# Kernel tuning notes

Measured on AMD Instinct MI355X. Metric: run time of the kernel, lower is better.

Reference implementation:

```python
import jax, jax.numpy as jnp
import numpy as np

B, C, L = 8, 512, 2048   # batch, input_dim (channels), sequence length
H = 8                    # multihead_cnt
K = 3                    # kernel_dim
DH = C // H              # per-head dim = 64
SCALE = 1.0 / float(np.sqrt(C))  # module divides by sqrt(input_dim), not sqrt(head_dim)


def _conv1d(x, w, b):
    # x: [B, C, L], w: [C_out, C_in, K], padding=1 keeps L
    y = jax.lax.conv_general_dilated(x, w, window_strides=(1,), padding=[(1, 1)],
                                     dimension_numbers=('NCH', 'OIH', 'NCH'))
    return y + b[None, :, None]


def setup_inputs() -> dict:
    key = jax.random.key(0)
    ks = jax.random.split(key, 7)
    x = jax.random.normal(ks[0], (B, C, L), dtype=jnp.float32)
    # xavier_normal_ std for Conv1d weight [C, C, K]: sqrt(2 / (fan_in + fan_out)), fan = C*K
    std = float(np.sqrt(2.0 / (C * K + C * K)))
    inp = {'x': x}
    for i in range(3):  # conv_cnt = 3 -> q, k, v convolutions
        inp[f'w{i}'] = jax.random.normal(ks[1 + 2 * i], (C, C, K), dtype=jnp.float32) * std
        inp[f'b{i}'] = jax.random.normal(ks[2 + 2 * i], (C,), dtype=jnp.float32) * 0.01
    return inp


def reference(x, w0, b0, w1, b1, w2, b2):
    # q, k, v projections via Conv1d (padding preserves length)
    q = _conv1d(x, w0, b0)  # [B, C, L]
    k = _conv1d(x, w1, b1)
    v = _conv1d(x, w2, b2)
    # torch.chunk along dim 1 == contiguous reshape into heads
    qh = q.reshape(B, H, DH, L)
    kh = k.reshape(B, H, DH, L)
    vh = v.reshape(B, H, DH, L)
    # scores = q^T k / sqrt(input_dim)  -> [B, H, L, L]
    scores = jnp.einsum('bhdl,bhdm->bhlm', qh, kh) * SCALE
    att = jax.nn.softmax(scores, axis=-1)
    # out = (att @ v^T)^T -> [B, H, DH, L]
    out = jnp.einsum('bhlm,bhdm->bhdl', att, vh)
    return out.reshape(B, C, L)
```

## Files before the change

kernel.cpp:

```cpp
#include <hip/hip_runtime.h>
#include <hip/hip_bf16.h>
#include <cstdint>

typedef unsigned short u16;
typedef short v8s __attribute__((ext_vector_type(8)));
typedef float v4f __attribute__((ext_vector_type(4)));
typedef u16 u16x8 __attribute__((ext_vector_type(8)));
typedef u16 u16x4 __attribute__((ext_vector_type(4)));

static constexpr int Bb = 8, Cc = 512, Ll = 2048, Hh = 8, Dh = 64;

__device__ __forceinline__ float bf2f(u16 u){
  unsigned x = ((unsigned)u) << 16; float f; __builtin_memcpy(&f, &x, 4); return f;
}
__device__ __forceinline__ u16 f2bf(float f){
  unsigned x; __builtin_memcpy(&x, &f, 4);
  x = (x + 0x7fffu + ((x >> 16) & 1u)) >> 16; return (u16)x;
}

__device__ __forceinline__ void async_cp16(const u16* g, u16* l){
  __builtin_amdgcn_global_load_lds(
      (const __attribute__((address_space(1))) unsigned int*)g,
      (__attribute__((address_space(3))) unsigned int*)l, 16, 0, 0);
}

#if __has_builtin(__builtin_amdgcn_exp2f)
#define EXP2F(x) __builtin_amdgcn_exp2f(x)
#else
#define EXP2F(x) exp2f(x)
#endif

__global__ __launch_bounds__(256) void detect_dtype(const u16* __restrict__ x, unsigned* __restrict__ flag){
  __shared__ int cnt;
  if (threadIdx.x == 0) cnt = 0;
  __syncthreads();
  int sane = 0;
  for (int i = threadIdx.x; i < 4096; i += 256){
    unsigned e = (x[2 * i] >> 7) & 0xFFu;
    sane += (e >= 90u && e <= 160u) ? 1 : 0;
  }
  atomicAdd(&cnt, sane);
  __syncthreads();
  if (threadIdx.x == 0) *flag = (cnt < 2458) ? 1u : 0u;
}

__global__ __launch_bounds__(256) void transpose_pad(const void* __restrict__ xv, const unsigned* __restrict__ flagp,
                                                     u16* __restrict__ xT){
  int b = blockIdx.z, ci0 = blockIdx.y * 64, l0 = blockIdx.x * 64;
  __shared__ u16 tb[64 * 72];
  const unsigned isf32 = *flagp;
  int t = threadIdx.x;
  int row = t >> 3, seg = t & 7;
  if (isf32){
    const float* xf = (const float*)xv;
    #pragma unroll
    for (int rnd = 0; rnd < 2; rnd++){
      int ci = row + rnd * 32;
      size_t off = ((size_t)(b * Cc + ci0 + ci)) * Ll + l0 + seg * 8;
      v4f a = *(const v4f*)(xf + off);
      v4f c4 = *(const v4f*)(xf + off + 4);
      #pragma unroll
      for (int j = 0; j < 4; j++) tb[(seg * 8 + j) * 72 + ci] = f2bf(a[j]);
      #pragma unroll
      for (int j = 0; j < 4; j++) tb[(seg * 8 + 4 + j) * 72 + ci] = f2bf(c4[j]);
    }
  } else {
    const u16* x = (const u16*)xv;
    #pragma unroll
    for (int rnd = 0; rnd < 2; rnd++){
      int ci = row + rnd * 32;
      u16x8 v = *(const u16x8*)(x + ((size_t)(b * Cc + ci0 + ci)) * Ll + l0 + seg * 8);
      #pragma unroll
      for (int j = 0; j < 8; j++) tb[(seg * 8 + j) * 72 + ci] = v[j];
    }
  }
  __syncthreads();
  #pragma unroll
  for (int rnd = 0; rnd < 2; rnd++){
    int l = row + rnd * 32;
    u16x8 v = *(const u16x8*)&tb[l * 72 + seg * 8];
    *(u16x8*)(xT + ((size_t)b * 2050 + 1 + l0 + l) * Cc + ci0 + seg * 8) = v;
  }
  if (blockIdx.x == 0 && t < 8){
    u16x8 z = {};
    *(u16x8*)(xT + ((size_t)b * 2050 + 0) * Cc + ci0 + t * 8) = z;
  }
  if (blockIdx.x == 31 && t < 8){
    u16x8 z = {};
    *(u16x8*)(xT + ((size_t)b * 2050 + 2049) * Cc + ci0 + t * 8) = z;
  }
}

__global__ __launch_bounds__(256) void pack_wb(const void* __restrict__ w0, const void* __restrict__ w1,
                                               const void* __restrict__ w2, const void* __restrict__ b0,
                                               const void* __restrict__ b1, const void* __restrict__ b2,
                                               const unsigned* __restrict__ flagp,
                                               u16* __restrict__ wp, u16* __restrict__ bb){
  int g = blockIdx.x * 256 + threadIdx.x;
  const unsigned isf32 = *flagp;
  if (g < 9 * 512 * 512){
    int ci = g & 511, co = (g >> 9) & 511, kc = g >> 18;
    int conv = kc / 3, k = kc - conv * 3;
    const void* w = (conv == 0) ? w0 : ((conv == 1) ? w1 : w2);
    size_t idx = (size_t)co * 1536 + ci * 3 + k;
    wp[g] = isf32 ? f2bf(((const float*)w)[idx]) : ((const u16*)w)[idx];
  } else {
    int g2 = g - 9 * 512 * 512;
    if (g2 < 1536){
      int conv = g2 >> 9, c = g2 & 511;
      const void* bsrc = (conv == 0) ? b0 : ((conv == 1) ? b1 : b2);
      bb[g2] = isf32 ? f2bf(((const float*)bsrc)[c]) : ((const u16*)bsrc)[c];
    }
  }
}

__global__ __launch_bounds__(256) void conv_gemm_fused(const u16* __restrict__ wp, const u16* __restrict__ xT,
                                                       const u16* __restrict__ bb, u16* __restrict__ qT,
                                                       u16* __restrict__ kT, u16* __restrict__ vN){
  int b = blockIdx.y, bx = blockIdx.x;
  int mt = bx >> 3, nt = bx & 7;
  int m0 = mt * 128, n0 = nt * 256;
  int conv = m0 >> 9;
  int co0 = m0 & 511;
  __shared__ u16 smem[12288 + 8256];
  u16* lA = smem;
  u16* lB = smem + 12288;
  int t = threadIdx.x, wave = t >> 6, lane = t & 63, quad = lane >> 4, lid = lane & 15;
  int wm = (wave >> 1) * 64, wn = (wave & 1) * 128;
  v4f acc[4][8] = {};
  const size_t xbase = (size_t)b * 2050 * Cc;

  for (int it = 0; it < 16; it++){
    int ci0 = it << 5;
    #pragma unroll
    for (int r = 0; r < 4; r++){
      int e = (r * 256 + t) * 8;
      int row = e >> 5, cio = e & 31;
      async_cp16(xT + xbase + (size_t)(n0 + row) * 512 + ci0 + cio, &lB[e]);
    }
    #pragma unroll
    for (int r = 0; r < 6; r++){
      int e = (r * 256 + t) * 8;
      int ks = e >> 12, rem = e & 4095, row = rem >> 5, cio = rem & 31;
      async_cp16(wp + ((size_t)((conv * 3 + ks) * 512 + co0 + row)) * 512 + ci0 + cio, &lA[e]);
    }
    if (t < 8){
      int hr = 256 + (t >> 2), cio = (t & 3) * 8;
      u16x8 hv = *(const u16x8*)(xT + xbase + (size_t)(n0 + hr) * 512 + ci0 + cio);
      *(u16x8*)&lB[hr * 32 + cio] = hv;
    }
    __syncthreads();
    #pragma unroll
    for (int ks = 0; ks < 3; ks++){
      v8s aF[4], bF[8];
      #pragma unroll
      for (int i = 0; i < 4; i++) aF[i] = *(const v8s*)&lA[ks * 4096 + (wm + i * 16 + lid) * 32 + quad * 8];
      #pragma unroll
      for (int j = 0; j < 8; j++) bF[j] = *(const v8s*)&lB[(wn + j * 16 + lid + ks) * 32 + quad * 8];
      #pragma unroll
      for (int i = 0; i < 4; i++)
        #pragma unroll
        for (int j = 0; j < 8; j++)
          acc[i][j] = __builtin_amdgcn_mfma_f32_16x16x32_bf16(aF[i], bF[j], acc[i][j], 0, 0, 0);
    }
    __syncthreads();
  }

  const float qsc = (float)(1.4426950408889634 / 22.627416997969522);
  if (conv < 2){
    u16* dst = (conv == 0) ? qT : kT;
    #pragma unroll
    for (int i = 0; i < 4; i++){
      int cog = m0 + wm + i * 16 + quad * 4;
      float bv[4];
      #pragma unroll
      for (int r = 0; r < 4; r++) bv[r] = bf2f(bb[cog + r]);
      int co = cog & 511;
      #pragma unroll
      for (int j = 0; j < 8; j++){
        int l = n0 + wn + j * 16 + lid;
        u16x4 pk;
        #pragma unroll
        for (int r = 0; r < 4; r++){
          float v = acc[i][j][r] + bv[r];
          if (conv == 0) v *= qsc;
          pk[r] = f2bf(v);
        }
        *(u16x4*)(dst + ((((size_t)b * Hh + (co >> 6)) * Ll + l) << 6) + (co & 63)) = pk;
      }
    }
  } else {
    u16* scr = smem;
    #pragma unroll
    for (int cs = 0; cs < 2; cs++){
      __syncthreads();
      #pragma unroll
      for (int i = 0; i < 4; i++){
        int cog = m0 + wm + i * 16 + quad * 4;
        float bv[4];
        #pragma unroll
        for (int r = 0; r < 4; r++) bv[r] = bf2f(bb[cog + r]);
        #pragma unroll
        for (int j = 0; j < 4; j++){
          int jj = cs * 4 + j;
          int lcl = (wave & 1) * 64 + j * 16 + lid;
          #pragma unroll
          for (int r = 0; r < 4; r++)
            scr[(wm + i * 16 + quad * 4 + r) * 130 + lcl] = f2bf(acc[i][jj][r] + bv[r]);
        }
      }
      __syncthreads();
      int row = t & 127, half = t >> 7;
      int co = co0 + row;
      size_t gb = (((size_t)b * Cc + co) << 11) + n0 + half * 128 + cs * 64;
      #pragma unroll
      for (int s = 0; s < 8; s++){
        u16x8 vv = *(const u16x8*)&scr[row * 130 + half * 64 + s * 8];
        *(u16x8*)(vN + gb + s * 8) = vv;
      }
    }
  }
}

__global__ __launch_bounds__(256) void attn_kernel(const u16* __restrict__ qT, const u16* __restrict__ kT,
                                                   const u16* __restrict__ vN, const unsigned* __restrict__ flagp,
                                                   void* __restrict__ outv){
  int bhx = blockIdx.x;
  int b = bhx >> 3, h = bhx & 7, l0 = blockIdx.y * 128;
  int t = threadIdx.x, w = t >> 6, lane = t & 63, quad = lane >> 4, lid = lane & 15;
  __shared__ u16 kls[128 * 72];
  __shared__ u16 vls[64 * 136];
  const unsigned isf32 = *flagp;
  const size_t bh = (size_t)b * Hh + h;

  int kadd[5], vadd[5];
  bool kval[5], vval[5];
  #pragma unroll
  for (int r = 0; r < 5; r++){
    int e = (r * 256 + t) * 8;
    kval[r] = e < 128 * 72;
    int slot = e / 72, off = e - slot * 72;
    int s5 = slot & 31;
    int m = (slot & ~31) | (((s5 >> 2) & 1) << 3) | (((s5 >> 3) & 1) << 4) | (((s5 >> 4) & 1) << 2) | (s5 & 3);
    kadd[r] = m * 64 + (off < 64 ? off : 0);
    vval[r] = e < 64 * 136;
    int d = e / 136, voff = e - d * 136;
    vadd[r] = d * Ll + (voff < 128 ? voff : 0);
  }
  const u16* kTb = kT + bh * Ll * 64;
  const u16* vNb = vN + ((size_t)(b * Cc + h * Dh)) * Ll;

  v8s qF[2][2];
  #pragma unroll
  for (int ci = 0; ci < 2; ci++)
    #pragma unroll
    for (int ks = 0; ks < 2; ks++)
      qF[ci][ks] = *(const v8s*)(qT + ((bh * Ll) + l0 + w * 32 + ci * 16 + lid) * 64 + ks * 32 + quad * 8);

  const v8s onesF = {0x3F80, 0x3F80, 0x3F80, 0x3F80, 0x3F80, 0x3F80, 0x3F80, 0x3F80};
  v4f o[2][4] = {};
  v4f o1[2] = {};

  for (int mt = 0; mt < 16; mt++){
    int m0 = mt * 128;
    const u16* kt = kTb + (size_t)m0 * 64;
    const u16* vt = vNb + m0;
    #pragma unroll
    for (int r = 0; r < 5; r++)
      if (kval[r]) async_cp16(kt + kadd[r], &kls[(r * 256 + t) * 8]);
    #pragma unroll
    for (int r = 0; r < 5; r++)
      if (vval[r]) async_cp16(vt + vadd[r], &vls[(r * 256 + t) * 8]);
    __syncthreads();

    v4f s[4][2][2] = {};
    #pragma unroll
    for (int ks = 0; ks < 2; ks++){
      v8s aF[4][2];
      #pragma unroll
      for (int c = 0; c < 4; c++)
        #pragma unroll
        for (int tt = 0; tt < 2; tt++)
          aF[c][tt] = *(const v8s*)&kls[(c * 32 + tt * 16 + lid) * 72 + ks * 32 + quad * 8];
      #pragma unroll
      for (int c = 0; c < 4; c++)
        #pragma unroll
        for (int tt = 0; tt < 2; tt++){
          s[c][tt][0] = __builtin_amdgcn_mfma_f32_16x16x32_bf16(aF[c][tt], qF[0][ks], s[c][tt][0], 0, 0, 0);
          s[c][tt][1] = __builtin_amdgcn_mfma_f32_16x16x32_bf16(aF[c][tt], qF[1][ks], s[c][tt][1], 0, 0, 0);
        }
    }

    #pragma unroll
    for (int c = 0; c < 4; c++){
      v8s aP[2];
      #pragma unroll
      for (int ci = 0; ci < 2; ci++){
        float p[8];
        #pragma unroll
        for (int tt = 0; tt < 2; tt++)
          #pragma unroll
          for (int r = 0; r < 4; r++)
            p[tt * 4 + r] = EXP2F(s[c][tt][ci][r]);
        unsigned u[4];
        #pragma unroll
        for (int k2 = 0; k2 < 4; k2++){
          __hip_bfloat162 hb = __float22bfloat162_rn(make_float2(p[2 * k2], p[2 * k2 + 1]));
          __builtin_memcpy(&u[k2], &hb, 4);
        }
        __builtin_memcpy(&aP[ci], u, 16);
      }
      v8s bV[4];
      #pragma unroll
      for (int df = 0; df < 4; df++)
        bV[df] = *(const v8s*)&vls[(df * 16 + lid) * 136 + c * 32 + quad * 8];
      #pragma unroll
      for (int ci = 0; ci < 2; ci++){
        #pragma unroll
        for (int df = 0; df < 4; df++)
          o[ci][df] = __builtin_amdgcn_mfma_f32_16x16x32_bf16(aP[ci], bV[df], o[ci][df], 0, 0, 0);
        o1[ci] = __builtin_amdgcn_mfma_f32_16x16x32_bf16(aP[ci], onesF, o1[ci], 0, 0, 0);
      }
    }
    __syncthreads();
  }

  #pragma unroll
  for (int lf = 0; lf < 2; lf++){
    v4f nv;
    #pragma unroll
    for (int r = 0; r < 4; r++) nv[r] = 1.f / o1[lf][r];
    #pragma unroll
    for (int df = 0; df < 4; df++){
      int d = df * 16 + lid;
      int l = l0 + w * 32 + lf * 16 + quad * 4;
      size_t ofs = (((bh << 6) + d) << 11) + l;
      if (isf32){
        v4f st;
        #pragma unroll
        for (int r = 0; r < 4; r++) st[r] = o[lf][df][r] * nv[r];
        *(v4f*)((float*)outv + ofs) = st;
      } else {
        u16x4 pk;
        #pragma unroll
        for (int r = 0; r < 4; r++) pk[r] = f2bf(o[lf][df][r] * nv[r]);
        *(u16x4*)((u16*)outv + ofs) = pk;
      }
    }
  }
}

extern "C" void kernel_launch(void* const* d_in, const int* in_sizes, int n_in,
                              void* d_out, int out_size, void* d_ws, size_t ws_size,
                              hipStream_t stream){
  const void* x  = d_in[0];
  const void* w0 = d_in[1];
  const void* b0 = d_in[2];
  const void* w1 = d_in[3];
  const void* b1 = d_in[4];
  const void* w2 = d_in[5];
  const void* b2 = d_in[6];
  u16* ws = (u16*)d_ws;
  unsigned* flag = (unsigned*)ws;
  u16* xT = ws + 64;
  u16* wp = xT + (size_t)8 * 2050 * 512;
  u16* bb = wp + (size_t)9 * 512 * 512;
  u16* qT = bb + 1536;
  u16* kT = qT + (size_t)8 * 8 * 2048 * 64;
  u16* vN = kT + (size_t)8 * 8 * 2048 * 64;

  detect_dtype<<<1, 256, 0, stream>>>((const u16*)x, flag);
  transpose_pad<<<dim3(32, 8, 8), 256, 0, stream>>>(x, flag, xT);
  pack_wb<<<dim3(9 * 512 * 512 / 256 + 6), 256, 0, stream>>>(w0, w1, w2, b0, b1, b2, flag, wp, bb);
  conv_gemm_fused<<<dim3(96, 8), 256, 0, stream>>>(wp, xT, bb, qT, kT, vN);
  attn_kernel<<<dim3(64, 16), 256, 0, stream>>>(qT, kT, vN, flag, d_out);
}
```

Measured before the change: 299.3 us.

## Rewrite conv GEMM as 256x256 tile, 512-thread double-buffered pipelined kernel

The conv-as-GEMM kernel moves from a 128x256 tile with 256 threads and a synchronous per-iteration load/compute loop to a 256x256 tile with 512 threads. It stages 64-wide K chunks into double-buffered LDS with an XOR swizzle and interleaves async global-to-LDS copies with four MFMA phases per iteration, using explicit waitcnt, s_barrier and setprio. The goal is to hide memory latency, raise data reuse per tile and avoid LDS bank conflicts. The cost is 128KB of LDS per block and heavier register pressure, which can limit occupancy. The grid is flattened with batch as the fastest-varying index, and the output staging is adjusted to the new tile shape.

Result: faster. 285.8 us (-4.5%).

```diff
diff --git a/kernel.cpp b/kernel.cpp
--- a/kernel.cpp
+++ b/kernel.cpp
@@ -114,109 +114,177 @@
   }
 }
 
-__global__ __launch_bounds__(256) void conv_gemm_fused(const u16* __restrict__ wp, const u16* __restrict__ xT,
-                                                       const u16* __restrict__ bb, u16* __restrict__ qT,
-                                                       u16* __restrict__ kT, u16* __restrict__ vN){
-  int b = blockIdx.y, bx = blockIdx.x;
-  int mt = bx >> 3, nt = bx & 7;
-  int m0 = mt * 128, n0 = nt * 256;
-  int conv = m0 >> 9;
-  int co0 = m0 & 511;
-  __shared__ u16 smem[12288 + 8256];
-  u16* lA = smem;
-  u16* lB = smem + 12288;
+__global__ __launch_bounds__(512, 2) void conv_gemm_fused(const u16* __restrict__ wp, const u16* __restrict__ xT,
+                                                          const u16* __restrict__ bb, u16* __restrict__ qT,
+                                                          u16* __restrict__ kT, u16* __restrict__ vN){
+  __shared__ u16 smem[65536];
+  int bx = blockIdx.x;
+  int b = bx & 7, inner = bx >> 3;
+  int mt = inner >> 3, nt = inner & 7;
+  int m0 = mt << 8, n0 = nt << 8;
+  int conv = m0 >> 9, co0 = m0 & 511;
+
   int t = threadIdx.x, wave = t >> 6, lane = t & 63, quad = lane >> 4, lid = lane & 15;
-  int wm = (wave >> 1) * 64, wn = (wave & 1) * 128;
-  v4f acc[4][8] = {};
-  const size_t xbase = (size_t)b * 2050 * Cc;
-
-  for (int it = 0; it < 16; it++){
-    int ci0 = it << 5;
-    #pragma unroll
-    for (int r = 0; r < 4; r++){
-      int e = (r * 256 + t) * 8;
-      int row = e >> 5, cio = e & 31;
-      async_cp16(xT + xbase + (size_t)(n0 + row) * 512 + ci0 + cio, &lB[e]);
-    }
-    #pragma unroll
-    for (int r = 0; r < 6; r++){
-      int e = (r * 256 + t) * 8;
-      int ks = e >> 12, rem = e & 4095, row = rem >> 5, cio = rem & 31;
-      async_cp16(wp + ((size_t)((conv * 3 + ks) * 512 + co0 + row)) * 512 + ci0 + cio, &lA[e]);
-    }
-    if (t < 8){
-      int hr = 256 + (t >> 2), cio = (t & 3) * 8;
-      u16x8 hv = *(const u16x8*)(xT + xbase + (size_t)(n0 + hr) * 512 + ci0 + cio);
-      *(u16x8*)&lB[hr * 32 + cio] = hv;
-    }
-    __syncthreads();
-    #pragma unroll
-    for (int ks = 0; ks < 3; ks++){
-      v8s aF[4], bF[8];
-      #pragma unroll
-      for (int i = 0; i < 4; i++) aF[i] = *(const v8s*)&lA[ks * 4096 + (wm + i * 16 + lid) * 32 + quad * 8];
-      #pragma unroll
-      for (int j = 0; j < 8; j++) bF[j] = *(const v8s*)&lB[(wn + j * 16 + lid + ks) * 32 + quad * 8];
-      #pragma unroll
-      for (int i = 0; i < 4; i++)
-        #pragma unroll
-        for (int j = 0; j < 8; j++)
-          acc[i][j] = __builtin_amdgcn_mfma_f32_16x16x32_bf16(aF[i], bF[j], acc[i][j], 0, 0, 0);
-    }
-    __syncthreads();
-  }
+  int wm_i = wave >> 2, wn_i = wave & 3;
+
+  int sx = ((lid & 1) << 6) | ((lid & 6) << 3);
+  int cb0 = ((quad * 16) ^ sx) >> 1;
+  int cb1 = ((64 + quad * 16) ^ sx) >> 1;
+  int abase0 = (wm_i * 64 + lid) * 64;
+  int bbase0 = 16384 + (wn_i * 32 + lid) * 64;
+
+  int p0 = t * 16, p1 = p0 + 8192;
+  int c0 = (p0 & 127) ^ ((((p0 >> 7) & 1) << 6) | (((p0 >> 8) & 1) << 4) | (((p0 >> 9) & 1) << 5));
+  int c1 = (p1 & 127) ^ ((((p1 >> 7) & 1) << 6) | (((p1 >> 8) & 1) << 4) | (((p1 >> 9) & 1) << 5));
+  int srcE0 = (p0 >> 7) * 512 + (c0 >> 1);
+  int srcE1 = (p1 >> 7) * 512 + (c1 >> 1);
+  int d0 = t * 8, d1 = 4096 + t * 8;
+
+  const u16* aGbase = wp + (size_t)(conv * 1536 + co0) * 512;
+  const u16* bGbase = xT + (size_t)b * (2050 * 512) + (size_t)n0 * 512;
+
+#define STAGE_HALF(gsrc, ldst) do{ \
+    async_cp16((gsrc) + srcE0, (ldst) + d0); \
+    async_cp16((gsrc) + srcE1, (ldst) + d1); }while(0)
+
+#define PHASE_WAIT() do{ \
+    asm volatile("s_waitcnt lgkmcnt(0)" ::: "memory"); \
+    __builtin_amdgcn_sched_barrier(0); \
+    __builtin_amdgcn_s_barrier(); }while(0)
+
+#define LOAD_A(mh) do{ \
+    _Pragma("unroll") for (int m = 0; m < 4; ++m){ \
+      af[m][0] = *(const v8s*)(lds + abase0 + (mh) * 8192 + m * 1024 + cb0); \
+      af[m][1] = *(const v8s*)(lds + abase0 + (mh) * 8192 + m * 1024 + cb1); } }while(0)
+
+#define LOAD_B(nh) do{ \
+    _Pragma("unroll") for (int n = 0; n < 2; ++n){ \
+      bf[n][0] = *(const v8s*)(lds + bbase0 + (nh) * 8192 + n * 1024 + cb0); \
+      bf[n][1] = *(const v8s*)(lds + bbase0 + (nh) * 8192 + n * 1024 + cb1); } }while(0)
+
+#define DO_MFMA(mh, nh) do{ \
+    __builtin_amdgcn_s_setprio(1); \
+    _Pragma("unroll") for (int m = 0; m < 4; ++m) \
+    _Pragma("unroll") for (int n = 0; n < 2; ++n) \
+    _Pragma("unroll") for (int kh = 0; kh < 2; ++kh) \
+      acc[mh][nh][m][n] = __builtin_amdgcn_mfma_f32_16x16x32_bf16(af[m][kh], bf[n][kh], acc[mh][nh][m][n], 0, 0, 0); \
+    __builtin_amdgcn_s_setprio(0); }while(0)
+
+  v4f acc[2][2][4][2] = {};
+  v8s af[4][2];
+
+  #pragma unroll
+  for (int k0 = 0; k0 < 2; ++k0){
+    u16* stg = smem + k0 * 32768;
+    const u16* aG = aGbase + k0 * 64;
+    const u16* bG = bGbase + k0 * 64;
+    STAGE_HALF(aG, stg);
+    STAGE_HALF(aG + 65536, stg + 8192);
+    STAGE_HALF(bG, stg + 16384);
+    STAGE_HALF(bG + 65536, stg + 24576);
+  }
+  asm volatile("s_waitcnt vmcnt(8)" ::: "memory");
+  __builtin_amdgcn_sched_barrier(0);
+  __builtin_amdgcn_s_barrier();
+
+  #pragma unroll 2
+  for (int kt = 0; kt < 24; ++kt){
+    u16* lds = smem + (kt & 1) * 32768;
+    u16* stg = lds;
+    int ks2 = (kt + 2) >> 3, ci2 = ((kt + 2) & 7) << 6;
+    const u16* aG = aGbase + (size_t)ks2 * 262144 + ci2;
+    const u16* bG = bGbase + (size_t)ks2 * 512 + ci2;
+    bool st = (kt < 22);
+    v8s bf[2][2];
+
+    LOAD_A(0); LOAD_B(0);
+    PHASE_WAIT();
+    DO_MFMA(0, 0);
+    LOAD_B(1);
+    if (st) STAGE_HALF(aG, stg);
+    PHASE_WAIT();
+    DO_MFMA(0, 1);
+    LOAD_A(1); LOAD_B(0);
+    PHASE_WAIT();
+    DO_MFMA(1, 0);
+    LOAD_B(1);
+    if (st){ STAGE_HALF(bG, stg + 16384); STAGE_HALF(aG + 65536, stg + 8192); }
+    PHASE_WAIT();
+    DO_MFMA(1, 1);
+    if (st){
+      STAGE_HALF(bG + 65536, stg + 24576);
+      asm volatile("s_waitcnt vmcnt(8)" ::: "memory");
+    } else if (kt == 22){
+      asm volatile("s_waitcnt vmcnt(0)" ::: "memory");
+    }
+    if (kt < 23){
+      __builtin_amdgcn_sched_barrier(0);
+      __builtin_amdgcn_s_barrier();
+    }
+  }
+
+#undef STAGE_HALF
+#undef PHASE_WAIT
+#undef LOAD_A
+#undef LOAD_B
+#undef DO_MFMA
 
   const float qsc = (float)(1.4426950408889634 / 22.627416997969522);
   if (conv < 2){
     u16* dst = (conv == 0) ? qT : kT;
     #pragma unroll
-    for (int i = 0; i < 4; i++){
-      int cog = m0 + wm + i * 16 + quad * 4;
+    for (int mh = 0; mh < 2; ++mh)
+    #pragma unroll
+    for (int m = 0; m < 4; ++m){
+      int cog = m0 + mh * 128 + wm_i * 64 + m * 16 + quad * 4;
       float bv[4];
       #pragma unroll
       for (int r = 0; r < 4; r++) bv[r] = bf2f(bb[cog + r]);
-      int co = cog & 511;
-      #pragma unroll
-      for (int j = 0; j < 8; j++){
-        int l = n0 + wn + j * 16 + lid;
+      int coc = cog & 511;
+      #pragma unroll
+      for (int nh = 0; nh < 2; ++nh)
+      #pragma unroll
+      for (int n = 0; n < 2; ++n){
+        int l = n0 + nh * 128 + wn_i * 32 + n * 16 + lid;
         u16x4 pk;
         #pragma unroll
         for (int r = 0; r < 4; r++){
-          float v = acc[i][j][r] + bv[r];
+          float v = acc[mh][nh][m][n][r] + bv[r];
           if (conv == 0) v *= qsc;
           pk[r] = f2bf(v);
         }
-        *(u16x4*)(dst + ((((size_t)b * Hh + (co >> 6)) * Ll + l) << 6) + (co & 63)) = pk;
+        *(u16x4*)(dst + ((((size_t)b * Hh + (coc >> 6)) * Ll + l) << 6) + (coc & 63)) = pk;
       }
     }
   } else {
     u16* scr = smem;
     #pragma unroll
-    for (int cs = 0; cs < 2; cs++){
+    for (int nh = 0; nh < 2; ++nh){
       __syncthreads();
       #pragma unroll
-      for (int i = 0; i < 4; i++){
-        int cog = m0 + wm + i * 16 + quad * 4;
+      for (int mh = 0; mh < 2; ++mh)
+      #pragma unroll
+      for (int m = 0; m < 4; ++m){
+        int rloc = mh * 128 + wm_i * 64 + m * 16 + quad * 4;
+        int cog = m0 + rloc;
         float bv[4];
         #pragma unroll
         for (int r = 0; r < 4; r++) bv[r] = bf2f(bb[cog + r]);
         #pragma unroll
-        for (int j = 0; j < 4; j++){
-          int jj = cs * 4 + j;
-          int lcl = (wave & 1) * 64 + j * 16 + lid;
+        for (int n = 0; n < 2; ++n){
+          int lcl = wn_i * 32 + n * 16 + lid;
           #pragma unroll
           for (int r = 0; r < 4; r++)
-            scr[(wm + i * 16 + quad * 4 + r) * 130 + lcl] = f2bf(acc[i][jj][r] + bv[r]);
+            scr[(rloc + r) * 132 + lcl] = f2bf(acc[mh][nh][m][n][r] + bv[r]);
         }
       }
       __syncthreads();
-      int row = t & 127, half = t >> 7;
-      int co = co0 + row;
-      size_t gb = (((size_t)b * Cc + co) << 11) + n0 + half * 128 + cs * 64;
-      #pragma unroll
-      for (int s = 0; s < 8; s++){
-        u16x8 vv = *(const u16x8*)&scr[row * 130 + half * 64 + s * 8];
-        *(u16x8*)(vN + gb + s * 8) = vv;
+      int seg = t & 15, rw = t >> 4;
+      #pragma unroll
+      for (int ps = 0; ps < 8; ++ps){
+        int row = rw + ps * 32;
+        u16x8 vv = *(const u16x8*)&scr[row * 132 + seg * 8];
+        *(u16x8*)(vN + (((size_t)b * Cc + co0 + row) << 11) + n0 + nh * 128 + seg * 8) = vv;
       }
     }
   }
@@ -372,6 +440,6 @@
   detect_dtype<<<1, 256, 0, stream>>>((const u16*)x, flag);
   transpose_pad<<<dim3(32, 8, 8), 256, 0, stream>>>(x, flag, xT);
   pack_wb<<<dim3(9 * 512 * 512 / 256 + 6), 256, 0, stream>>>(w0, w1, w2, b0, b1, b2, flag, wp, bb);
-  conv_gemm_fused<<<dim3(96, 8), 256, 0, stream>>>(wp, xT, bb, qT, kT, vN);
+  conv_gemm_fused<<<dim3(384), 512, 0, stream>>>(wp, xT, bb, qT, kT, vN);
   attn_kernel<<<dim3(64, 16), 256, 0, stream>>>(qT, kT, vN, flag, d_out);
 }
```
